# Performance work log

Measured on AMD Instinct MI355X. Metric: run time of the kernel, lower is better.

The kernel has to match this reference:

```python
import jax, jax.numpy as jnp
import numpy as np

SIM_T = 0.2       # similarity_threshold
AMB_T = 0.17      # ambiguous_threshold
SPLIT = 24576     # split_size
CAP = 65536       # fixed capacity per split for compacted pairs (padded with -1)


def _l2norm(x):
    # F.normalize(p=2, dim=1) with eps clamp
    n = jnp.linalg.norm(x, axis=1, keepdims=True)
    return x / jnp.maximum(n, 1e-12)


def setup_inputs():
    key = jax.random.key(0)
    ks = jax.random.split(key, 8)
    N1, N2, D = 4096, 49152, 512
    features = jax.random.normal(ks[0], (N1, D), dtype=jnp.float32)
    labels = jax.random.randint(ks[1], (N1,), 0, 10000, dtype=jnp.int32)
    counts = jax.random.randint(ks[2], (N1,), 0, 100, dtype=jnp.int32)
    indexes = jax.random.randint(ks[3], (N1,), 0, N2, dtype=jnp.int32)
    features_db = jax.random.normal(ks[4], (N2, D), dtype=jnp.float32)
    labels_db = jax.random.randint(ks[5], (N2,), 0, 10000, dtype=jnp.int32)
    counts_db = jax.random.randint(ks[6], (N2,), 0, 100, dtype=jnp.int32)
    indexes_db = jnp.arange(N2, dtype=jnp.int32)
    return {
        "features": features, "labels": labels, "counts": counts, "indexes": indexes,
        "features_db": features_db, "labels_db": labels_db,
        "counts_db": counts_db, "indexes_db": indexes_db,
    }


def reference(features, labels, counts, indexes,
              features_db, labels_db, counts_db, indexes_db):
    f1 = _l2norm(features)                        # [N1, D]
    f2 = _l2norm(features_db)                     # [N2, D]
    n_splits = features_db.shape[0] // SPLIT      # static small loop (2)
    ar = jnp.arange(CAP)
    similar_pairs, ambiguous_pairs = [], []
    for s in range(n_splits):
        sl = slice(s * SPLIT, (s + 1) * SPLIT)
        f2s, l2, c2, i2 = f2[sl], labels_db[sl], counts_db[sl], indexes_db[sl]
        sim = f1 @ f2s.T                          # [N1, SPLIT] cosine similarity
        # validity mask: global_idx1 < global_idx2 AND different labels
        valid = (indexes[:, None] < i2[None, :]) & (labels[:, None] != l2[None, :])
        # ---- similar pairs (sim > SIM_T) ----
        m = (sim > SIM_T) & valid
        r, c = jnp.nonzero(m, size=CAP, fill_value=0)   # fixed-size compaction
        good = ar < jnp.sum(m)
        p = jnp.stack([labels[r], l2[c]], axis=1)       # [CAP, 2] label pairs
        similar_pairs.append(jnp.where(good[:, None], p, -1))
        # ---- ambiguous pairs (AMB_T < sim < SIM_T), sorted by counts ----
        ma = (sim > AMB_T) & (sim < SIM_T) & valid
        r, c = jnp.nonzero(ma, size=CAP, fill_value=0)
        good = ar < jnp.sum(ma)
        p = jnp.stack([labels[r], l2[c]], axis=1)
        swap = counts[r] > c2[c]                        # argsort of 2-elem counts
        p = jnp.where(swap[:, None], p[:, ::-1], p)
        ambiguous_pairs.append(jnp.where(good[:, None], p, -1))
    similar_pairs = jnp.concatenate(similar_pairs, axis=0)     # [n_splits*CAP, 2]
    ambiguous_pairs = jnp.concatenate(ambiguous_pairs, axis=0) # [n_splits*CAP, 2]
    return similar_pairs, ambiguous_pairs
```

## Files before the change

### kernel.cpp

```cpp
#include <hip/hip_runtime.h>

typedef unsigned long long u64;

#define N1c 4096
#define N2c 49152
#define Dc 512
#define SPLITc 24576
#define NSPLITc 2
#define CAPc 65536
#define WPSc (SPLITc / 64)
#define SIM_Tc 0.2f
#define AMB_Tc 0.17f
#define DELTAc 0.01f
#define CANDMAX (1 << 20)

typedef __bf16 bf16x8 __attribute__((ext_vector_type(8)));
typedef float f32x4 __attribute__((ext_vector_type(4)));

static __device__ __forceinline__ unsigned short f2bf(float x) {
  unsigned u = __float_as_uint(x);
  unsigned r = (u + 0x7fffu + ((u >> 16) & 1u)) >> 16;
  return (unsigned short)r;
}

__global__ void sim_fill_out_k(int* __restrict__ out, int n) {
  int i = blockIdx.x * blockDim.x + threadIdx.x;
  if (i < n) out[i] = -1;
}

__global__ void sim_zero_k(int* __restrict__ p) { if (threadIdx.x == 0) *p = 0; }

__global__ void sim_norm_k(const float* __restrict__ f1, const float* __restrict__ f2,
                           float* __restrict__ invn, unsigned short* __restrict__ f1nb) {
  int wid = threadIdx.x >> 6, lane = threadIdx.x & 63;
  int row = blockIdx.x * 4 + wid;
  if (row >= N1c + N2c) return;
  const float* src = (row < N1c) ? (f1 + (size_t)row * Dc)
                                 : (f2 + (size_t)(row - N1c) * Dc);
  const float4* p = (const float4*)src;
  float4 v0 = p[lane];
  float4 v1 = p[lane + 64];
  float ss = v0.x*v0.x + v0.y*v0.y + v0.z*v0.z + v0.w*v0.w
           + v1.x*v1.x + v1.y*v1.y + v1.z*v1.z + v1.w*v1.w;
  #pragma unroll
  for (int d = 1; d < 64; d <<= 1) ss += __shfl_xor(ss, d);
  float inv = 1.0f / fmaxf(sqrtf(ss), 1e-12f);
  if (lane == 0) invn[row] = inv;
  if (row < N1c) {
    ushort4 o0, o1;
    o0.x = f2bf(v0.x*inv); o0.y = f2bf(v0.y*inv); o0.z = f2bf(v0.z*inv); o0.w = f2bf(v0.w*inv);
    o1.x = f2bf(v1.x*inv); o1.y = f2bf(v1.y*inv); o1.z = f2bf(v1.z*inv); o1.w = f2bf(v1.w*inv);
    ushort4* q = (ushort4*)(f1nb + (size_t)row * Dc);
    q[lane] = o0; q[lane + 64] = o1;
  }
}

__global__ void sim_conv2_k(const float* __restrict__ f2, const float* __restrict__ invn,
                            unsigned short* __restrict__ f2nb, int s) {
  int wid = threadIdx.x >> 6, lane = threadIdx.x & 63;
  int rloc = blockIdx.x * 4 + wid;
  if (rloc >= SPLITc) return;
  int grow = s * SPLITc + rloc;
  float inv = invn[N1c + grow];
  const float4* p = (const float4*)(f2 + (size_t)grow * Dc);
  float4 v0 = p[lane];
  float4 v1 = p[lane + 64];
  ushort4 o0, o1;
  o0.x = f2bf(v0.x*inv); o0.y = f2bf(v0.y*inv); o0.z = f2bf(v0.z*inv); o0.w = f2bf(v0.w*inv);
  o1.x = f2bf(v1.x*inv); o1.y = f2bf(v1.y*inv); o1.z = f2bf(v1.z*inv); o1.w = f2bf(v1.w*inv);
  ushort4* q = (ushort4*)(f2nb + (size_t)rloc * Dc);
  q[lane] = o0; q[lane + 64] = o1;
}

__global__ __launch_bounds__(256, 2) void sim_mfma_k(
    const unsigned short* __restrict__ Abf, const unsigned short* __restrict__ Bbf,
    const int* __restrict__ labels, const int* __restrict__ indexes,
    const int* __restrict__ labels_db, const int* __restrict__ indexes_db,
    u64* __restrict__ msim, u64* __restrict__ mamb,
    unsigned* __restrict__ cands, int* __restrict__ ccount, int s)
{
  __shared__ unsigned short As[128 * 64];
  __shared__ unsigned short Bs[128 * 64];
  __shared__ u64 wS[128][2];
  __shared__ u64 wA[128][2];

  const int tid  = threadIdx.x;
  const int lane = tid & 63;
  const int wid  = tid >> 6;
  const int wm   = wid >> 1, wn = wid & 1;
  const int rbase = blockIdx.y * 128;
  const int cbase = blockIdx.x * 128;

  f32x4 acc[4][4];
  #pragma unroll
  for (int i = 0; i < 4; ++i)
    #pragma unroll
    for (int j = 0; j < 4; ++j) acc[i][j] = (f32x4){0.f, 0.f, 0.f, 0.f};

  for (int kb = 0; kb < Dc; kb += 64) {
    __syncthreads();
    #pragma unroll
    for (int c4 = 0; c4 < 4; ++c4) {
      int c   = wid * 4 + c4;
      int row = c * 8 + (lane >> 3);
      int ls  = (lane & 7) ^ (row & 7);
      const unsigned short* ga = Abf + (size_t)(rbase + row) * Dc + kb + ls * 8;
      const unsigned short* gb = Bbf + (size_t)(cbase + row) * Dc + kb + ls * 8;
      __builtin_amdgcn_global_load_lds((const __attribute__((address_space(1))) void*)ga,
          (__attribute__((address_space(3))) void*)(As + c * 512), 16, 0, 0);
      __builtin_amdgcn_global_load_lds((const __attribute__((address_space(1))) void*)gb,
          (__attribute__((address_space(3))) void*)(Bs + c * 512), 16, 0, 0);
    }
    __syncthreads();
    #pragma unroll
    for (int kk = 0; kk < 2; ++kk) {
      bf16x8 a[4], b[4];
      #pragma unroll
      for (int mi = 0; mi < 4; ++mi) {
        int r  = wm * 64 + mi * 16 + (lane & 15);
        int ps = (kk * 4 + (lane >> 4)) ^ (r & 7);
        a[mi] = *(const bf16x8*)(const void*)(As + r * 64 + ps * 8);
      }
      #pragma unroll
      for (int ni = 0; ni < 4; ++ni) {
        int r  = wn * 64 + ni * 16 + (lane & 15);
        int ps = (kk * 4 + (lane >> 4)) ^ (r & 7);
        b[ni] = *(const bf16x8*)(const void*)(Bs + r * 64 + ps * 8);
      }
      #pragma unroll
      for (int mi = 0; mi < 4; ++mi)
        #pragma unroll
        for (int ni = 0; ni < 4; ++ni)
          acc[mi][ni] = __builtin_amdgcn_mfma_f32_16x16x32_bf16(a[mi], b[ni], acc[mi][ni], 0, 0, 0);
    }
  }

  wS[tid >> 1][tid & 1] = 0;
  wA[tid >> 1][tid & 1] = 0;
  __syncthreads();

  int lab2[4], idx2[4], cloc[4];
  #pragma unroll
  for (int ni = 0; ni < 4; ++ni) {
    cloc[ni] = cbase + wn * 64 + ni * 16 + (lane & 15);
    int gc = s * SPLITc + cloc[ni];
    lab2[ni] = labels_db[gc];
    idx2[ni] = indexes_db[gc];
  }

  #pragma unroll
  for (int mi = 0; mi < 4; ++mi) {
    #pragma unroll
    for (int r = 0; r < 4; ++r) {
      int row128 = wm * 64 + mi * 16 + (lane >> 4) * 4 + r;
      int gr = rbase + row128;
      int lab1 = labels[gr], idx1 = indexes[gr];
      u64 sb = 0, ab = 0;
      #pragma unroll
      for (int ni = 0; ni < 4; ++ni) {
        float v = acc[mi][ni][r];
        if (idx1 < idx2[ni] && lab1 != lab2[ni]) {
          if (v > SIM_Tc + DELTAc) {
            sb |= 1ull << (ni * 16 + (lane & 15));
          } else if (v > AMB_Tc - DELTAc) {
            if (v < SIM_Tc - DELTAc && v > AMB_Tc + DELTAc) {
              ab |= 1ull << (ni * 16 + (lane & 15));
            } else {
              int ci = atomicAdd(ccount, 1);
              if (ci < CANDMAX)
                cands[ci] = ((unsigned)gr << 15) | (unsigned)cloc[ni];
            }
          }
        }
      }
      if (sb) atomicOr(&wS[row128][wn], sb);
      if (ab) atomicOr(&wA[row128][wn], ab);
    }
  }
  __syncthreads();
  {
    int row128 = tid >> 1, jh = tid & 1;
    size_t w = (size_t)(rbase + row128) * WPSc + (cbase >> 6) + jh;
    msim[w] = wS[row128][jh];
    mamb[w] = wA[row128][jh];
  }
}

__global__ void sim_recheck_k(const float* __restrict__ f1, const float* __restrict__ f2,
                              const float* __restrict__ invn,
                              const unsigned* __restrict__ cands, const int* __restrict__ ccount,
                              u64* __restrict__ msim, u64* __restrict__ mamb, int s) {
  int lane = threadIdx.x & 63;
  int gw = (blockIdx.x * blockDim.x + threadIdx.x) >> 6;
  int nw = (gridDim.x * blockDim.x) >> 6;
  int n = *ccount; if (n > CANDMAX) n = CANDMAX;
  for (int i = gw; i < n; i += nw) {
    unsigned pk = cands[i];
    int r = (int)(pk >> 15), c = (int)(pk & 0x7fffu);
    const float4* pa = (const float4*)(f1 + (size_t)r * Dc);
    const float4* pb = (const float4*)(f2 + ((size_t)s * SPLITc + c) * Dc);
    float4 a0 = pa[lane], a1 = pa[lane + 64];
    float4 b0 = pb[lane], b1 = pb[lane + 64];
    float d = a0.x*b0.x + a0.y*b0.y + a0.z*b0.z + a0.w*b0.w
            + a1.x*b1.x + a1.y*b1.y + a1.z*b1.z + a1.w*b1.w;
    #pragma unroll
    for (int t = 1; t < 64; t <<= 1) d += __shfl_xor(d, t);
    if (lane == 0) {
      float v = d * invn[r] * invn[N1c + s * SPLITc + c];
      if (v > SIM_Tc)
        atomicOr(&msim[(size_t)r * WPSc + (c >> 6)], 1ull << (c & 63));
      else if (v > AMB_Tc)
        atomicOr(&mamb[(size_t)r * WPSc + (c >> 6)], 1ull << (c & 63));
    }
  }
}

__global__ void sim_rowcount_k(const u64* __restrict__ msim, const u64* __restrict__ mamb,
                               int* __restrict__ rowcnt) {
  int row = blockIdx.x;
  int wid = threadIdx.x >> 6, lane = threadIdx.x & 63;
  const u64* m = wid ? mamb : msim;
  int ssum = 0;
  #pragma unroll
  for (int it = 0; it < WPSc / 64; ++it)
    ssum += __popcll(m[(size_t)row * WPSc + it * 64 + lane]);
  #pragma unroll
  for (int d = 32; d; d >>= 1) ssum += __shfl_down(ssum, d);
  if (lane == 0) rowcnt[wid * N1c + row] = ssum;
}

__global__ void sim_scan_k(const int* __restrict__ rowcnt, int* __restrict__ rowoff) {
  int cat = blockIdx.x;
  int tid = threadIdx.x;
  int v[16]; int ssum = 0;
  #pragma unroll
  for (int i = 0; i < 16; ++i) { v[i] = rowcnt[cat * N1c + tid * 16 + i]; ssum += v[i]; }
  int lane = tid & 63, wid = tid >> 6;
  int incl = ssum;
  #pragma unroll
  for (int d = 1; d < 64; d <<= 1) { int t = __shfl_up(incl, d); if (lane >= d) incl += t; }
  __shared__ int wsum[4];
  if (lane == 63) wsum[wid] = incl;
  __syncthreads();
  int woff = 0;
  for (int w = 0; w < wid; ++w) woff += wsum[w];
  int run = woff + incl - ssum;
  #pragma unroll
  for (int i = 0; i < 16; ++i) { rowoff[cat * N1c + tid * 16 + i] = run; run += v[i]; }
}

__global__ void sim_scatter_k(const u64* __restrict__ msim, const u64* __restrict__ mamb,
                              const int* __restrict__ rowoff,
                              const int* __restrict__ labels, const int* __restrict__ counts,
                              const int* __restrict__ labels_db, const int* __restrict__ counts_db,
                              int* __restrict__ out, int s) {
  int row = blockIdx.x;
  int cat = blockIdx.y;
  int lane = threadIdx.x;
  const u64* m = cat ? mamb : msim;
  int* o = out + (cat ? (NSPLITc * CAPc * 2 + s * CAPc * 2) : (s * CAPc * 2));
  int run = rowoff[cat * N1c + row];
  int lab1 = labels[row];
  int cnt1 = counts[row];
  for (int it = 0; it < WPSc / 64; ++it) {
    int w = it * 64 + lane;
    u64 x = m[(size_t)row * WPSc + w];
    int pc = __popcll(x);
    int incl = pc;
    #pragma unroll
    for (int d = 1; d < 64; d <<= 1) { int t = __shfl_up(incl, d); if (lane >= d) incl += t; }
    int pos = run + incl - pc;
    int tot = __shfl(incl, 63);
    while (x) {
      int b = __builtin_ctzll(x);
      x &= x - 1;
      if (pos < CAPc) {
        int gc = s * SPLITc + w * 64 + b;
        int l2v = labels_db[gc];
        if (cat == 0) {
          o[2 * pos]     = lab1;
          o[2 * pos + 1] = l2v;
        } else {
          bool sw = cnt1 > counts_db[gc];
          o[2 * pos]     = sw ? l2v : lab1;
          o[2 * pos + 1] = sw ? lab1 : l2v;
        }
      }
      ++pos;
    }
    run += tot;
  }
}

extern "C" void kernel_launch(void* const* d_in, const int* in_sizes, int n_in,
                              void* d_out, int out_size, void* d_ws, size_t ws_size,
                              hipStream_t stream) {
  const float* features    = (const float*)d_in[0];
  const int*   labels      = (const int*)  d_in[1];
  const int*   counts      = (const int*)  d_in[2];
  const int*   indexes     = (const int*)  d_in[3];
  const float* features_db = (const float*)d_in[4];
  const int*   labels_db   = (const int*)  d_in[5];
  const int*   counts_db   = (const int*)  d_in[6];
  const int*   indexes_db  = (const int*)  d_in[7];
  int* out = (int*)d_out;

  u64*   msim   = (u64*)d_ws;
  u64*   mamb   = msim + (size_t)N1c * WPSc;
  float* invn   = (float*)(mamb + (size_t)N1c * WPSc);
  int*   rowcnt = (int*)(invn + (N1c + N2c));
  int*   rowoff = rowcnt + 2 * N1c;
  int*   ccount = rowoff + 2 * N1c;
  unsigned* cands = (unsigned*)(ccount + 4);
  unsigned short* f1nb = (unsigned short*)(cands + CANDMAX);
  unsigned short* f2nb = f1nb + (size_t)N1c * Dc;

  sim_fill_out_k<<<(out_size + 255) / 256, 256, 0, stream>>>(out, out_size);
  sim_norm_k<<<(N1c + N2c + 3) / 4, 256, 0, stream>>>(features, features_db, invn, f1nb);

  for (int s = 0; s < NSPLITc; ++s) {
    sim_conv2_k<<<SPLITc / 4, 256, 0, stream>>>(features_db, invn, f2nb, s);
    sim_zero_k<<<1, 64, 0, stream>>>(ccount);
    sim_mfma_k<<<dim3(SPLITc / 128, N1c / 128), 256, 0, stream>>>(
        f1nb, f2nb, labels, indexes, labels_db, indexes_db,
        msim, mamb, cands, ccount, s);
    sim_recheck_k<<<512, 256, 0, stream>>>(features, features_db, invn,
                                           cands, ccount, msim, mamb, s);
    sim_rowcount_k<<<N1c, 128, 0, stream>>>(msim, mamb, rowcnt);
    sim_scan_k<<<2, 256, 0, stream>>>(rowcnt, rowoff);
    sim_scatter_k<<<dim3(N1c, 2), 64, 0, stream>>>(
        msim, mamb, rowoff, labels, counts, labels_db, counts_db, out, s);
  }
}
```

Before: 401.8 us.

## Enlarge GEMM tile to 256x256 with double-buffered LDS and fuse first-split bf16 conversion

The similarity GEMM moves from 128x128 tiles with 4 waves to 256x256 tiles with 8 waves, each wave computing a 128x64 sub-tile. The K loop now double-buffers the LDS stages so the next global-to-LDS load overlaps the current MFMA work, with one barrier per step. The norm kernel also writes the bf16 normalized rows for split 0 directly, so the separate conversion launch runs only for split 1. The larger tile needs 128 KB of LDS and many more accumulator registers, which can cut occupancy. The grid also shrinks to 96x16 blocks, which may load the CUs unevenly.

```diff
diff --git a/kernel.cpp b/kernel.cpp
--- a/kernel.cpp
+++ b/kernel.cpp
@@ -31,7 +31,8 @@
 __global__ void sim_zero_k(int* __restrict__ p) { if (threadIdx.x == 0) *p = 0; }
 
 __global__ void sim_norm_k(const float* __restrict__ f1, const float* __restrict__ f2,
-                           float* __restrict__ invn, unsigned short* __restrict__ f1nb) {
+                           float* __restrict__ invn, unsigned short* __restrict__ f1nb,
+                           unsigned short* __restrict__ f2nb) {
   int wid = threadIdx.x >> 6, lane = threadIdx.x & 63;
   int row = blockIdx.x * 4 + wid;
   if (row >= N1c + N2c) return;
@@ -46,11 +47,14 @@
   for (int d = 1; d < 64; d <<= 1) ss += __shfl_xor(ss, d);
   float inv = 1.0f / fmaxf(sqrtf(ss), 1e-12f);
   if (lane == 0) invn[row] = inv;
-  if (row < N1c) {
+  unsigned short* dst = 0;
+  if (row < N1c) dst = f1nb + (size_t)row * Dc;
+  else if (row < N1c + SPLITc) dst = f2nb + (size_t)(row - N1c) * Dc;
+  if (dst) {
     ushort4 o0, o1;
     o0.x = f2bf(v0.x*inv); o0.y = f2bf(v0.y*inv); o0.z = f2bf(v0.z*inv); o0.w = f2bf(v0.w*inv);
     o1.x = f2bf(v1.x*inv); o1.y = f2bf(v1.y*inv); o1.z = f2bf(v1.z*inv); o1.w = f2bf(v1.w*inv);
-    ushort4* q = (ushort4*)(f1nb + (size_t)row * Dc);
+    ushort4* q = (ushort4*)dst;
     q[lane] = o0; q[lane + 64] = o1;
   }
 }
@@ -72,72 +76,88 @@
   q[lane] = o0; q[lane + 64] = o1;
 }
 
-__global__ __launch_bounds__(256, 2) void sim_mfma_k(
+__global__ __launch_bounds__(512, 2) void sim_mfma_k(
     const unsigned short* __restrict__ Abf, const unsigned short* __restrict__ Bbf,
     const int* __restrict__ labels, const int* __restrict__ indexes,
     const int* __restrict__ labels_db, const int* __restrict__ indexes_db,
     u64* __restrict__ msim, u64* __restrict__ mamb,
     unsigned* __restrict__ cands, int* __restrict__ ccount, int s)
 {
-  __shared__ unsigned short As[128 * 64];
-  __shared__ unsigned short Bs[128 * 64];
-  __shared__ u64 wS[128][2];
-  __shared__ u64 wA[128][2];
+  __shared__ __align__(16) unsigned short As[2][256 * 64];
+  __shared__ __align__(16) unsigned short Bs[2][256 * 64];
+  __shared__ u64 wS[256][4];
+  __shared__ u64 wA[256][4];
 
   const int tid  = threadIdx.x;
   const int lane = tid & 63;
   const int wid  = tid >> 6;
-  const int wm   = wid >> 1, wn = wid & 1;
-  const int rbase = blockIdx.y * 128;
-  const int cbase = blockIdx.x * 128;
-
-  f32x4 acc[4][4];
-  #pragma unroll
-  for (int i = 0; i < 4; ++i)
+  const int wm   = wid >> 2;
+  const int wn   = wid & 3;
+  const int rbase = blockIdx.y * 256;
+  const int cbase = blockIdx.x * 256;
+
+  #pragma unroll
+  for (int i = 0; i < 2; ++i) {
+    int w = tid * 2 + i;
+    wS[w >> 2][w & 3] = 0;
+    wA[w >> 2][w & 3] = 0;
+  }
+
+  f32x4 acc[8][4];
+  #pragma unroll
+  for (int i = 0; i < 8; ++i)
     #pragma unroll
     for (int j = 0; j < 4; ++j) acc[i][j] = (f32x4){0.f, 0.f, 0.f, 0.f};
 
-  for (int kb = 0; kb < Dc; kb += 64) {
+#define STAGE_T(pb, kb) do {                                                     \
+    const int sub_ = lane >> 3, ps_ = lane & 7, ls_ = ps_ ^ sub_;                \
+    _Pragma("unroll")                                                            \
+    for (int i_ = 0; i_ < 4; ++i_) {                                             \
+      int row_ = i_ * 64 + wid * 8 + sub_;                                       \
+      const unsigned short* ga_ = Abf + (size_t)(rbase + row_) * Dc + (kb) + ls_ * 8; \
+      const unsigned short* gb_ = Bbf + (size_t)(cbase + row_) * Dc + (kb) + ls_ * 8; \
+      __builtin_amdgcn_global_load_lds(                                          \
+          (const __attribute__((address_space(1))) void*)ga_,                    \
+          (__attribute__((address_space(3))) void*)(&As[pb][i_ * 4096 + wid * 512]), \
+          16, 0, 0);                                                             \
+      __builtin_amdgcn_global_load_lds(                                          \
+          (const __attribute__((address_space(1))) void*)gb_,                    \
+          (__attribute__((address_space(3))) void*)(&Bs[pb][i_ * 4096 + wid * 512]), \
+          16, 0, 0);                                                             \
+    } } while (0)
+
+#define COMPUTE_T(pb) do {                                                       \
+    _Pragma("unroll")                                                            \
+    for (int kk_ = 0; kk_ < 2; ++kk_) {                                          \
+      bf16x8 a_[8], b_[4];                                                       \
+      _Pragma("unroll")                                                          \
+      for (int mi_ = 0; mi_ < 8; ++mi_) {                                        \
+        int r_  = wm * 128 + mi_ * 16 + (lane & 15);                             \
+        int ps_ = (kk_ * 4 + (lane >> 4)) ^ (r_ & 7);                            \
+        a_[mi_] = *(const bf16x8*)(const void*)(&As[pb][r_ * 64 + ps_ * 8]);     \
+      }                                                                          \
+      _Pragma("unroll")                                                          \
+      for (int ni_ = 0; ni_ < 4; ++ni_) {                                        \
+        int r_  = wn * 64 + ni_ * 16 + (lane & 15);                              \
+        int ps_ = (kk_ * 4 + (lane >> 4)) ^ (r_ & 7);                            \
+        b_[ni_] = *(const bf16x8*)(const void*)(&Bs[pb][r_ * 64 + ps_ * 8]);     \
+      }                                                                          \
+      _Pragma("unroll")                                                          \
+      for (int mi_ = 0; mi_ < 8; ++mi_)                                          \
+        _Pragma("unroll")                                                        \
+        for (int ni_ = 0; ni_ < 4; ++ni_)                                        \
+          acc[mi_][ni_] = __builtin_amdgcn_mfma_f32_16x16x32_bf16(               \
+              a_[mi_], b_[ni_], acc[mi_][ni_], 0, 0, 0);                         \
+    } } while (0)
+
+  STAGE_T(0, 0);
+  __syncthreads();
+  #pragma unroll
+  for (int t = 0; t < 8; ++t) {
+    if (t < 7) STAGE_T((t + 1) & 1, (t + 1) * 64);
+    COMPUTE_T(t & 1);
     __syncthreads();
-    #pragma unroll
-    for (int c4 = 0; c4 < 4; ++c4) {
-      int c   = wid * 4 + c4;
-      int row = c * 8 + (lane >> 3);
-      int ls  = (lane & 7) ^ (row & 7);
-      const unsigned short* ga = Abf + (size_t)(rbase + row) * Dc + kb + ls * 8;
-      const unsigned short* gb = Bbf + (size_t)(cbase + row) * Dc + kb + ls * 8;
-      __builtin_amdgcn_global_load_lds((const __attribute__((address_space(1))) void*)ga,
-          (__attribute__((address_space(3))) void*)(As + c * 512), 16, 0, 0);
-      __builtin_amdgcn_global_load_lds((const __attribute__((address_space(1))) void*)gb,
-          (__attribute__((address_space(3))) void*)(Bs + c * 512), 16, 0, 0);
-    }
-    __syncthreads();
-    #pragma unroll
-    for (int kk = 0; kk < 2; ++kk) {
-      bf16x8 a[4], b[4];
-      #pragma unroll
-      for (int mi = 0; mi < 4; ++mi) {
-        int r  = wm * 64 + mi * 16 + (lane & 15);
-        int ps = (kk * 4 + (lane >> 4)) ^ (r & 7);
-        a[mi] = *(const bf16x8*)(const void*)(As + r * 64 + ps * 8);
-      }
-      #pragma unroll
-      for (int ni = 0; ni < 4; ++ni) {
-        int r  = wn * 64 + ni * 16 + (lane & 15);
-        int ps = (kk * 4 + (lane >> 4)) ^ (r & 7);
-        b[ni] = *(const bf16x8*)(const void*)(Bs + r * 64 + ps * 8);
-      }
-      #pragma unroll
-      for (int mi = 0; mi < 4; ++mi)
-        #pragma unroll
-        for (int ni = 0; ni < 4; ++ni)
-          acc[mi][ni] = __builtin_amdgcn_mfma_f32_16x16x32_bf16(a[mi], b[ni], acc[mi][ni], 0, 0, 0);
-    }
-  }
-
-  wS[tid >> 1][tid & 1] = 0;
-  wA[tid >> 1][tid & 1] = 0;
-  __syncthreads();
+  }
 
   int lab2[4], idx2[4], cloc[4];
   #pragma unroll
@@ -149,16 +169,16 @@
   }
 
   #pragma unroll
-  for (int mi = 0; mi < 4; ++mi) {
+  for (int mi = 0; mi < 8; ++mi) {
     #pragma unroll
-    for (int r = 0; r < 4; ++r) {
-      int row128 = wm * 64 + mi * 16 + (lane >> 4) * 4 + r;
-      int gr = rbase + row128;
+    for (int rr = 0; rr < 4; ++rr) {
+      int row256 = wm * 128 + mi * 16 + (lane >> 4) * 4 + rr;
+      int gr = rbase + row256;
       int lab1 = labels[gr], idx1 = indexes[gr];
       u64 sb = 0, ab = 0;
       #pragma unroll
       for (int ni = 0; ni < 4; ++ni) {
-        float v = acc[mi][ni][r];
+        float v = acc[mi][ni][rr];
         if (idx1 < idx2[ni] && lab1 != lab2[ni]) {
           if (v > SIM_Tc + DELTAc) {
             sb |= 1ull << (ni * 16 + (lane & 15));
@@ -173,17 +193,21 @@
           }
         }
       }
-      if (sb) atomicOr(&wS[row128][wn], sb);
-      if (ab) atomicOr(&wA[row128][wn], ab);
+      if (sb) atomicOr(&wS[row256][wn], sb);
+      if (ab) atomicOr(&wA[row256][wn], ab);
     }
   }
   __syncthreads();
-  {
-    int row128 = tid >> 1, jh = tid & 1;
-    size_t w = (size_t)(rbase + row128) * WPSc + (cbase >> 6) + jh;
-    msim[w] = wS[row128][jh];
-    mamb[w] = wA[row128][jh];
-  }
+  #pragma unroll
+  for (int i = 0; i < 2; ++i) {
+    int w = tid * 2 + i;
+    int row = w >> 2, jh = w & 3;
+    size_t widx = (size_t)(rbase + row) * WPSc + (cbase >> 6) + jh;
+    msim[widx] = wS[row][jh];
+    mamb[widx] = wA[row][jh];
+  }
+#undef STAGE_T
+#undef COMPUTE_T
 }
 
 __global__ void sim_recheck_k(const float* __restrict__ f1, const float* __restrict__ f2,
@@ -316,12 +340,12 @@
   unsigned short* f2nb = f1nb + (size_t)N1c * Dc;
 
   sim_fill_out_k<<<(out_size + 255) / 256, 256, 0, stream>>>(out, out_size);
-  sim_norm_k<<<(N1c + N2c + 3) / 4, 256, 0, stream>>>(features, features_db, invn, f1nb);
+  sim_norm_k<<<(N1c + N2c + 3) / 4, 256, 0, stream>>>(features, features_db, invn, f1nb, f2nb);
 
   for (int s = 0; s < NSPLITc; ++s) {
-    sim_conv2_k<<<SPLITc / 4, 256, 0, stream>>>(features_db, invn, f2nb, s);
+    if (s) sim_conv2_k<<<SPLITc / 4, 256, 0, stream>>>(features_db, invn, f2nb, s);
     sim_zero_k<<<1, 64, 0, stream>>>(ccount);
-    sim_mfma_k<<<dim3(SPLITc / 128, N1c / 128), 256, 0, stream>>>(
+    sim_mfma_k<<<dim3(SPLITc / 256, N1c / 256), 512, 0, stream>>>(
         f1nb, f2nb, labels, indexes, labels_db, indexes_db,
         msim, mamb, cands, ccount, s);
     sim_recheck_k<<<512, 256, 0, stream>>>(features, features_db, invn,
```

New measurement: 477.2 us. 1.19x slower.
